# Optimization experiments

Measured on AMD Instinct MI355X. Metric: run time of the kernel, lower is better.

The kernel has to match this reference:

```python
import jax, jax.numpy as jnp
import numpy as np


def setup_inputs() -> dict:
    key = jax.random.key(0)
    k1, k2, k3 = jax.random.split(key, 3)
    B, C, L, D = 2, 8, 256, 128
    start_hidden = jax.random.normal(k1, (B, C, L, D), dtype=jnp.float32)
    end_hidden = jax.random.normal(k2, (B, C, L, D), dtype=jnp.float32)
    # nn.Parameter initialized uniform_(-0.1, 0.1)
    v = jax.random.uniform(k3, (D,), dtype=jnp.float32, minval=-0.1, maxval=0.1)
    return {"start_hidden": start_hidden, "end_hidden": end_hidden, "v": v}


def reference(start_hidden, end_hidden, v):
    # start_hidden: [B, C, L, D], end_hidden: [B, C, L, D], v: [D]
    # additive pairwise scoring: tanh(s_i + e_j) . v  for every (i, j) span
    add_hidden = jnp.tanh(start_hidden[:, :, :, None, :] + end_hidden[:, :, None, :, :])  # [B,C,L,L,D]
    res = jnp.einsum('bcnmd,d->bcnm', add_hidden, v)  # [B, C, L, L]
    span_ner_mat_tensor = jnp.transpose(res, (0, 2, 3, 1))  # [B, L, L, C]
    return span_ner_mat_tensor
```

## Files before the change

### kernel.cpp

```cpp
#include <hip/hip_runtime.h>


#define LDIM 256
#define DDIM 128
#define DPAD 132

__global__ __launch_bounds__(256) void span_tanh_dot_kernel(
    const float* __restrict__ start_h,
    const float* __restrict__ end_h,
    const float* __restrict__ v,
    float* __restrict__ out,
    int C)
{
    __shared__ float s_pool[32 * DPAD];
    __shared__ float e_t[32][DPAD];
    __shared__ float s_vsum;
    float (*s_t)[DPAD] = (float (*)[DPAD])s_pool;

    const int bc = blockIdx.z;
    const int i0 = blockIdx.y * 32;
    const int j0 = blockIdx.x * 32;
    const int tx = threadIdx.x;
    const int ty = threadIdx.y;
    const int g  = threadIdx.z;
    const int t  = ty * 8 + tx;
    const int tid = g * 64 + t;

    const float K = 2.8853900817779268f;

    const float* sg = start_h + ((size_t)bc * LDIM + i0) * DDIM;
    const float* eg = end_h   + ((size_t)bc * LDIM + j0) * DDIM;

    #pragma unroll
    for (int k = 0; k < 4; ++k) {
        const int idx = tid + k * 256;
        const int r  = idx >> 5;
        const int c4 = (idx & 31) << 2;
        const float4 vv = *(const float4*)(v + c4);
        const float w0 = __builtin_amdgcn_rcpf(vv.x);
        const float w1 = __builtin_amdgcn_rcpf(vv.y);
        const float w2 = __builtin_amdgcn_rcpf(vv.z);
        const float w3 = __builtin_amdgcn_rcpf(vv.w);
        float4 a = *(const float4*)(sg + r * DDIM + c4);
        a.x = __builtin_amdgcn_exp2f(K * a.x) * w0;
        a.y = __builtin_amdgcn_exp2f(K * a.y) * w1;
        a.z = __builtin_amdgcn_exp2f(K * a.z) * w2;
        a.w = __builtin_amdgcn_exp2f(K * a.w) * w3;
        *(float4*)(&s_t[r][c4]) = a;
        float4 b = *(const float4*)(eg + r * DDIM + c4);
        b.x = __builtin_amdgcn_exp2f(K * b.x);
        b.y = __builtin_amdgcn_exp2f(K * b.y);
        b.z = __builtin_amdgcn_exp2f(K * b.z);
        b.w = __builtin_amdgcn_exp2f(K * b.w);
        *(float4*)(&e_t[r][c4]) = b;
    }

    if (tid < 128) {
        s_t[tid >> 2][128 + (tid & 3)] = __builtin_amdgcn_rcpf(v[tid]);
    }

    if (g == 0) {
        float2 vv = *(const float2*)(v + 2 * t);
        float p = vv.x + vv.y;
        #pragma unroll
        for (int off = 1; off < 64; off <<= 1) p += __shfl_xor(p, off);
        if (t == 0) s_vsum = p;
    }
    __syncthreads();

    const int g8 = __builtin_amdgcn_readfirstlane(g) * 8;

    float acc00 = 0.f, acc01 = 0.f, acc02 = 0.f, acc03 = 0.f;
    float acc10 = 0.f, acc11 = 0.f, acc12 = 0.f, acc13 = 0.f;
    float acc20 = 0.f, acc21 = 0.f, acc22 = 0.f, acc23 = 0.f;
    float acc30 = 0.f, acc31 = 0.f, acc32 = 0.f, acc33 = 0.f;

#define QUAD(ACC, S, E)                                            \
    {                                                              \
        float u0 = fmaf((S).x, (E).x, W.x);                        \
        float u1 = fmaf((S).y, (E).y, W.y);                        \
        float u2 = fmaf((S).z, (E).z, W.z);                        \
        float u3 = fmaf((S).w, (E).w, W.w);                        \
        float ab = u0 * u1, cd = u2 * u3;                          \
        float n01 = u0 + u1;                                       \
        float n23 = u2 + u3;                                       \
        float N = fmaf(n01, cd, n23 * ab);                         \
        float r = __builtin_amdgcn_rcpf(ab * cd);                  \
        ACC = fmaf(N, r, ACC);                                     \
    }

    #pragma unroll 2
    for (int it = 0; it < 8; ++it) {
        const int d = (g8 + it) * 4;
        const float4 W  = *(const float4*)(&s_t[g8 + it][128]);
        const float4 s0 = *(const float4*)(&s_t[ty     ][d]);
        const float4 s1 = *(const float4*)(&s_t[ty +  8][d]);
        const float4 s2 = *(const float4*)(&s_t[ty + 16][d]);
        const float4 s3 = *(const float4*)(&s_t[ty + 24][d]);
        const float4 e0 = *(const float4*)(&e_t[tx     ][d]);
        const float4 e1 = *(const float4*)(&e_t[tx +  8][d]);
        const float4 e2 = *(const float4*)(&e_t[tx + 16][d]);
        const float4 e3 = *(const float4*)(&e_t[tx + 24][d]);

        QUAD(acc00, s0, e0); QUAD(acc01, s0, e1); QUAD(acc02, s0, e2); QUAD(acc03, s0, e3);
        QUAD(acc10, s1, e0); QUAD(acc11, s1, e1); QUAD(acc12, s1, e2); QUAD(acc13, s1, e3);
        QUAD(acc20, s2, e0); QUAD(acc21, s2, e1); QUAD(acc22, s2, e2); QUAD(acc23, s2, e3);
        QUAD(acc30, s3, e0); QUAD(acc31, s3, e1); QUAD(acc32, s3, e2); QUAD(acc33, s3, e3);
    }
#undef QUAD

    __syncthreads();
    float* red = s_pool;
#define PARK(A, B, ACC) red[(((A) * 4 + (B)) * 4 + g) * 64 + t] = ACC;
    PARK(0,0,acc00) PARK(0,1,acc01) PARK(0,2,acc02) PARK(0,3,acc03)
    PARK(1,0,acc10) PARK(1,1,acc11) PARK(1,2,acc12) PARK(1,3,acc13)
    PARK(2,0,acc20) PARK(2,1,acc21) PARK(2,2,acc22) PARK(2,3,acc23)
    PARK(3,0,acc30) PARK(3,1,acc31) PARK(3,2,acc32) PARK(3,3,acc33)
#undef PARK
    __syncthreads();

#define COMB(B)                                                    \
    (red[((g * 4 + (B)) * 4 + 0) * 64 + t] +                       \
     red[((g * 4 + (B)) * 4 + 1) * 64 + t] +                       \
     red[((g * 4 + (B)) * 4 + 2) * 64 + t] +                       \
     red[((g * 4 + (B)) * 4 + 3) * 64 + t])
    const float o0 = COMB(0);
    const float o1 = COMB(1);
    const float o2 = COMB(2);
    const float o3 = COMB(3);
#undef COMB

    const int b_ = bc / C;
    const int c_ = bc - b_ * C;
    const float Sv = s_vsum;
    const int i = i0 + ty + 8 * g;
    const size_t rowbase = (((size_t)b_ * LDIM + i) * LDIM) * C + c_;
    out[rowbase + (size_t)(j0 + tx     ) * C] = fmaf(-2.f, o0, Sv);
    out[rowbase + (size_t)(j0 + tx +  8) * C] = fmaf(-2.f, o1, Sv);
    out[rowbase + (size_t)(j0 + tx + 16) * C] = fmaf(-2.f, o2, Sv);
    out[rowbase + (size_t)(j0 + tx + 24) * C] = fmaf(-2.f, o3, Sv);
}

extern "C" void kernel_launch(void* const* d_in, const int* in_sizes, int n_in,
                              void* d_out, int out_size, void* d_ws, size_t ws_size,
                              hipStream_t stream) {
    const float* start_h = (const float*)d_in[0];
    const float* end_h   = (const float*)d_in[1];
    const float* v       = (const float*)d_in[2];
    float* out = (float*)d_out;

    const int BC = in_sizes[0] / (LDIM * DDIM);
    const int C  = 8;

    dim3 grid(LDIM / 32, LDIM / 32, BC);
    dim3 block(8, 8, 4);
    span_tanh_dot_kernel<<<grid, block, 0, stream>>>(start_h, end_h, v, out, C);
}
```

Baseline: 18.34 us.

## Enlarge block tile to 64x64 with 1024 threads and fold scaling into W

Each block now covers a 64x64 (i,j) tile using 16 wavefronts arranged as 4 quadrants by 4 D-slices. Each exponentiated start/end row is loaded once per block and reused across twice as many pairs, which cuts redundant global loads and exp work. The -2 output scale and 1/v weights are folded into a separate shared W array, so the epilogue becomes a plain add. The trade-off is a 4x smaller grid (256 blocks) and larger LDS use per block, which may reduce occupancy and latency hiding.

```diff
diff --git a/kernel.cpp b/kernel.cpp
--- a/kernel.cpp
+++ b/kernel.cpp
@@ -5,61 +5,69 @@
 #define DDIM 128
 #define DPAD 132
 
-__global__ __launch_bounds__(256) void span_tanh_dot_kernel(
+__global__ __launch_bounds__(1024) void span_tanh_dot_kernel(
     const float* __restrict__ start_h,
     const float* __restrict__ end_h,
     const float* __restrict__ v,
     float* __restrict__ out,
     int C)
 {
-    __shared__ float s_pool[32 * DPAD];
-    __shared__ float e_t[32][DPAD];
+    __shared__ float pool[2 * 64 * DPAD];
+    __shared__ float W_s[DDIM];
     __shared__ float s_vsum;
-    float (*s_t)[DPAD] = (float (*)[DPAD])s_pool;
+
+    float* s_t = pool;
+    float* e_t = pool + 64 * DPAD;
 
     const int bc = blockIdx.z;
-    const int i0 = blockIdx.y * 32;
-    const int j0 = blockIdx.x * 32;
+    const int i0 = blockIdx.y * 64;
+    const int j0 = blockIdx.x * 64;
     const int tx = threadIdx.x;
     const int ty = threadIdx.y;
-    const int g  = threadIdx.z;
+    const int wz = threadIdx.z;
     const int t  = ty * 8 + tx;
-    const int tid = g * 64 + t;
+    const int tid = wz * 64 + t;
+
+    const int q  = wz & 3;
+    const int h  = wz >> 2;
+    const int qi = q >> 1, qj = q & 1;
 
     const float K = 2.8853900817779268f;
 
     const float* sg = start_h + ((size_t)bc * LDIM + i0) * DDIM;
     const float* eg = end_h   + ((size_t)bc * LDIM + j0) * DDIM;
 
+    if (tid < 32) {
+        const float4 vv = *(const float4*)(v + 4 * tid);
+        float4 w;
+        w.x = -0.5f * __builtin_amdgcn_rcpf(vv.x);
+        w.y = -0.5f * __builtin_amdgcn_rcpf(vv.y);
+        w.z = -0.5f * __builtin_amdgcn_rcpf(vv.z);
+        w.w = -0.5f * __builtin_amdgcn_rcpf(vv.w);
+        *(float4*)(&W_s[4 * tid]) = w;
+    }
+
     #pragma unroll
-    for (int k = 0; k < 4; ++k) {
-        const int idx = tid + k * 256;
+    for (int k = 0; k < 2; ++k) {
+        const int idx = tid + k * 1024;
         const int r  = idx >> 5;
         const int c4 = (idx & 31) << 2;
         const float4 vv = *(const float4*)(v + c4);
-        const float w0 = __builtin_amdgcn_rcpf(vv.x);
-        const float w1 = __builtin_amdgcn_rcpf(vv.y);
-        const float w2 = __builtin_amdgcn_rcpf(vv.z);
-        const float w3 = __builtin_amdgcn_rcpf(vv.w);
         float4 a = *(const float4*)(sg + r * DDIM + c4);
-        a.x = __builtin_amdgcn_exp2f(K * a.x) * w0;
-        a.y = __builtin_amdgcn_exp2f(K * a.y) * w1;
-        a.z = __builtin_amdgcn_exp2f(K * a.z) * w2;
-        a.w = __builtin_amdgcn_exp2f(K * a.w) * w3;
-        *(float4*)(&s_t[r][c4]) = a;
+        a.x = __builtin_amdgcn_exp2f(K * a.x) * (-0.5f * __builtin_amdgcn_rcpf(vv.x));
+        a.y = __builtin_amdgcn_exp2f(K * a.y) * (-0.5f * __builtin_amdgcn_rcpf(vv.y));
+        a.z = __builtin_amdgcn_exp2f(K * a.z) * (-0.5f * __builtin_amdgcn_rcpf(vv.z));
+        a.w = __builtin_amdgcn_exp2f(K * a.w) * (-0.5f * __builtin_amdgcn_rcpf(vv.w));
+        *(float4*)(&s_t[r * DPAD + c4]) = a;
         float4 b = *(const float4*)(eg + r * DDIM + c4);
         b.x = __builtin_amdgcn_exp2f(K * b.x);
         b.y = __builtin_amdgcn_exp2f(K * b.y);
         b.z = __builtin_amdgcn_exp2f(K * b.z);
         b.w = __builtin_amdgcn_exp2f(K * b.w);
-        *(float4*)(&e_t[r][c4]) = b;
+        *(float4*)(&e_t[r * DPAD + c4]) = b;
     }
 
-    if (tid < 128) {
-        s_t[tid >> 2][128 + (tid & 3)] = __builtin_amdgcn_rcpf(v[tid]);
-    }
-
-    if (g == 0) {
+    if (wz == 0) {
         float2 vv = *(const float2*)(v + 2 * t);
         float p = vv.x + vv.y;
         #pragma unroll
@@ -68,7 +76,9 @@
     }
     __syncthreads();
 
-    const int g8 = __builtin_amdgcn_readfirstlane(g) * 8;
+    const int dbase = __builtin_amdgcn_readfirstlane(h) * 32;
+    const float* srow = s_t + (qi * 32 + ty) * DPAD;
+    const float* erow = e_t + (qj * 32 + tx) * DPAD;
 
     float acc00 = 0.f, acc01 = 0.f, acc02 = 0.f, acc03 = 0.f;
     float acc10 = 0.f, acc11 = 0.f, acc12 = 0.f, acc13 = 0.f;
@@ -91,16 +101,16 @@
 
     #pragma unroll 2
     for (int it = 0; it < 8; ++it) {
-        const int d = (g8 + it) * 4;
-        const float4 W  = *(const float4*)(&s_t[g8 + it][128]);
-        const float4 s0 = *(const float4*)(&s_t[ty     ][d]);
-        const float4 s1 = *(const float4*)(&s_t[ty +  8][d]);
-        const float4 s2 = *(const float4*)(&s_t[ty + 16][d]);
-        const float4 s3 = *(const float4*)(&s_t[ty + 24][d]);
-        const float4 e0 = *(const float4*)(&e_t[tx     ][d]);
-        const float4 e1 = *(const float4*)(&e_t[tx +  8][d]);
-        const float4 e2 = *(const float4*)(&e_t[tx + 16][d]);
-        const float4 e3 = *(const float4*)(&e_t[tx + 24][d]);
+        const int d = dbase + it * 4;
+        const float4 W  = *(const float4*)(&W_s[d]);
+        const float4 s0 = *(const float4*)(srow + d);
+        const float4 s1 = *(const float4*)(srow +  8 * DPAD + d);
+        const float4 s2 = *(const float4*)(srow + 16 * DPAD + d);
+        const float4 s3 = *(const float4*)(srow + 24 * DPAD + d);
+        const float4 e0 = *(const float4*)(erow + d);
+        const float4 e1 = *(const float4*)(erow +  8 * DPAD + d);
+        const float4 e2 = *(const float4*)(erow + 16 * DPAD + d);
+        const float4 e3 = *(const float4*)(erow + 24 * DPAD + d);
 
         QUAD(acc00, s0, e0); QUAD(acc01, s0, e1); QUAD(acc02, s0, e2); QUAD(acc03, s0, e3);
         QUAD(acc10, s1, e0); QUAD(acc11, s1, e1); QUAD(acc12, s1, e2); QUAD(acc13, s1, e3);
@@ -110,20 +120,20 @@
 #undef QUAD
 
     __syncthreads();
-    float* red = s_pool;
-#define PARK(A, B, ACC) red[(((A) * 4 + (B)) * 4 + g) * 64 + t] = ACC;
-    PARK(0,0,acc00) PARK(0,1,acc01) PARK(0,2,acc02) PARK(0,3,acc03)
-    PARK(1,0,acc10) PARK(1,1,acc11) PARK(1,2,acc12) PARK(1,3,acc13)
-    PARK(2,0,acc20) PARK(2,1,acc21) PARK(2,2,acc22) PARK(2,3,acc23)
-    PARK(3,0,acc30) PARK(3,1,acc31) PARK(3,2,acc32) PARK(3,3,acc33)
-#undef PARK
+    float* park = pool;
+#define PK(A, B, ACC) park[((((q * 4 + h) * 4 + (A)) * 4 + (B)) * 64) + t] = ACC;
+    PK(0,0,acc00) PK(0,1,acc01) PK(0,2,acc02) PK(0,3,acc03)
+    PK(1,0,acc10) PK(1,1,acc11) PK(1,2,acc12) PK(1,3,acc13)
+    PK(2,0,acc20) PK(2,1,acc21) PK(2,2,acc22) PK(2,3,acc23)
+    PK(3,0,acc30) PK(3,1,acc31) PK(3,2,acc32) PK(3,3,acc33)
+#undef PK
     __syncthreads();
 
-#define COMB(B)                                                    \
-    (red[((g * 4 + (B)) * 4 + 0) * 64 + t] +                       \
-     red[((g * 4 + (B)) * 4 + 1) * 64 + t] +                       \
-     red[((g * 4 + (B)) * 4 + 2) * 64 + t] +                       \
-     red[((g * 4 + (B)) * 4 + 3) * 64 + t])
+#define COMB(B)                                                        \
+    (park[(((q * 4 + 0) * 4 + h) * 4 + (B)) * 64 + t] +                \
+     park[(((q * 4 + 1) * 4 + h) * 4 + (B)) * 64 + t] +                \
+     park[(((q * 4 + 2) * 4 + h) * 4 + (B)) * 64 + t] +                \
+     park[(((q * 4 + 3) * 4 + h) * 4 + (B)) * 64 + t])
     const float o0 = COMB(0);
     const float o1 = COMB(1);
     const float o2 = COMB(2);
@@ -133,12 +143,13 @@
     const int b_ = bc / C;
     const int c_ = bc - b_ * C;
     const float Sv = s_vsum;
-    const int i = i0 + ty + 8 * g;
+    const int i = i0 + qi * 32 + ty + 8 * h;
+    const int j = j0 + qj * 32 + tx;
     const size_t rowbase = (((size_t)b_ * LDIM + i) * LDIM) * C + c_;
-    out[rowbase + (size_t)(j0 + tx     ) * C] = fmaf(-2.f, o0, Sv);
-    out[rowbase + (size_t)(j0 + tx +  8) * C] = fmaf(-2.f, o1, Sv);
-    out[rowbase + (size_t)(j0 + tx + 16) * C] = fmaf(-2.f, o2, Sv);
-    out[rowbase + (size_t)(j0 + tx + 24) * C] = fmaf(-2.f, o3, Sv);
+    out[rowbase + (size_t)(j     ) * C] = Sv + o0;
+    out[rowbase + (size_t)(j +  8) * C] = Sv + o1;
+    out[rowbase + (size_t)(j + 16) * C] = Sv + o2;
+    out[rowbase + (size_t)(j + 24) * C] = Sv + o3;
 }
 
 extern "C" void kernel_launch(void* const* d_in, const int* in_sizes, int n_in,
@@ -152,7 +163,7 @@
     const int BC = in_sizes[0] / (LDIM * DDIM);
     const int C  = 8;
 
-    dim3 grid(LDIM / 32, LDIM / 32, BC);
-    dim3 block(8, 8, 4);
+    dim3 grid(LDIM / 64, LDIM / 64, BC);
+    dim3 block(8, 8, 16);
     span_tanh_dot_kernel<<<grid, block, 0, stream>>>(start_h, end_h, v, out, C);
 }
```

Result: slower. 19.55 us (+6.6%).

## Precompute exp tables in workspace and read them directly from global memory

Applied to the files above, without the earlier changes.

Adds a precompute kernel that writes exp(2x)/v-scaled start and exp(2x) end tables into the workspace, once per element instead of once per tile. The main kernel then drops its shared-memory staging and reads float4 operands straight from global/L2, and folds the -2 scaling into the weights. This removes the redundant exp work and one barrier, at the cost of an extra launch and about 4 MB of extra global traffic. Per-thread global loads in the inner loop may also have higher latency than LDS reads. A fallback kernel keeps the shared-memory path for when no workspace is available.

```diff
diff --git a/kernel.cpp b/kernel.cpp
--- a/kernel.cpp
+++ b/kernel.cpp
@@ -3,19 +3,49 @@
 
 #define LDIM 256
 #define DDIM 128
-#define DPAD 132
-
-__global__ __launch_bounds__(256) void span_tanh_dot_kernel(
-    const float* __restrict__ start_h,
-    const float* __restrict__ end_h,
+#define TBL_ELEMS (2 * 8 * 256 * 128)
+#define KLOG2E 2.8853900817779268f
+
+__global__ __launch_bounds__(256) void precompute_kernel(
+    const float* __restrict__ s_in,
+    const float* __restrict__ e_in,
+    const float* __restrict__ v,
+    float* __restrict__ ws)
+{
+    const int i = blockIdx.x * 256 + threadIdx.x;
+    const int c4 = (i & 31) << 2;
+    const float4 vv = *(const float4*)(v + c4);
+    const float w0 = -0.5f * __builtin_amdgcn_rcpf(vv.x);
+    const float w1 = -0.5f * __builtin_amdgcn_rcpf(vv.y);
+    const float w2 = -0.5f * __builtin_amdgcn_rcpf(vv.z);
+    const float w3 = -0.5f * __builtin_amdgcn_rcpf(vv.w);
+
+    float4 a = *(const float4*)(s_in + 4 * (size_t)i);
+    float4 o;
+    o.x = __builtin_amdgcn_exp2f(KLOG2E * a.x) * w0;
+    o.y = __builtin_amdgcn_exp2f(KLOG2E * a.y) * w1;
+    o.z = __builtin_amdgcn_exp2f(KLOG2E * a.z) * w2;
+    o.w = __builtin_amdgcn_exp2f(KLOG2E * a.w) * w3;
+    *(float4*)(ws + 4 * (size_t)i) = o;
+
+    float4 b = *(const float4*)(e_in + 4 * (size_t)i);
+    float4 p;
+    p.x = __builtin_amdgcn_exp2f(KLOG2E * b.x);
+    p.y = __builtin_amdgcn_exp2f(KLOG2E * b.y);
+    p.z = __builtin_amdgcn_exp2f(KLOG2E * b.z);
+    p.w = __builtin_amdgcn_exp2f(KLOG2E * b.w);
+    *(float4*)(ws + TBL_ELEMS + 4 * (size_t)i) = p;
+}
+
+__global__ __launch_bounds__(256) void span_main_kernel(
+    const float* __restrict__ ws,
     const float* __restrict__ v,
     float* __restrict__ out,
     int C)
 {
-    __shared__ float s_pool[32 * DPAD];
-    __shared__ float e_t[32][DPAD];
+    __shared__ float red[4096];
+    __shared__ float W_s[DDIM];
     __shared__ float s_vsum;
-    float (*s_t)[DPAD] = (float (*)[DPAD])s_pool;
 
     const int bc = blockIdx.z;
     const int i0 = blockIdx.y * 32;
@@ -26,39 +56,15 @@
     const int t  = ty * 8 + tx;
     const int tid = g * 64 + t;
 
-    const float K = 2.8853900817779268f;
-
-    const float* sg = start_h + ((size_t)bc * LDIM + i0) * DDIM;
-    const float* eg = end_h   + ((size_t)bc * LDIM + j0) * DDIM;
-
-    #pragma unroll
-    for (int k = 0; k < 4; ++k) {
-        const int idx = tid + k * 256;
-        const int r  = idx >> 5;
-        const int c4 = (idx & 31) << 2;
-        const float4 vv = *(const float4*)(v + c4);
-        const float w0 = __builtin_amdgcn_rcpf(vv.x);
-        const float w1 = __builtin_amdgcn_rcpf(vv.y);
-        const float w2 = __builtin_amdgcn_rcpf(vv.z);
-        const float w3 = __builtin_amdgcn_rcpf(vv.w);
-        float4 a = *(const float4*)(sg + r * DDIM + c4);
-        a.x = __builtin_amdgcn_exp2f(K * a.x) * w0;
-        a.y = __builtin_amdgcn_exp2f(K * a.y) * w1;
-        a.z = __builtin_amdgcn_exp2f(K * a.z) * w2;
-        a.w = __builtin_amdgcn_exp2f(K * a.w) * w3;
-        *(float4*)(&s_t[r][c4]) = a;
-        float4 b = *(const float4*)(eg + r * DDIM + c4);
-        b.x = __builtin_amdgcn_exp2f(K * b.x);
-        b.y = __builtin_amdgcn_exp2f(K * b.y);
-        b.z = __builtin_amdgcn_exp2f(K * b.z);
-        b.w = __builtin_amdgcn_exp2f(K * b.w);
-        *(float4*)(&e_t[r][c4]) = b;
-    }
-
-    if (tid < 128) {
-        s_t[tid >> 2][128 + (tid & 3)] = __builtin_amdgcn_rcpf(v[tid]);
-    }
-
+    if (tid < 32) {
+        const float4 vv = *(const float4*)(v + 4 * tid);
+        float4 w;
+        w.x = -0.5f * __builtin_amdgcn_rcpf(vv.x);
+        w.y = -0.5f * __builtin_amdgcn_rcpf(vv.y);
+        w.z = -0.5f * __builtin_amdgcn_rcpf(vv.z);
+        w.w = -0.5f * __builtin_amdgcn_rcpf(vv.w);
+        *(float4*)(&W_s[4 * tid]) = w;
+    }
     if (g == 0) {
         float2 vv = *(const float2*)(v + 2 * t);
         float p = vv.x + vv.y;
@@ -68,7 +74,9 @@
     }
     __syncthreads();
 
-    const int g8 = __builtin_amdgcn_readfirstlane(g) * 8;
+    const int dbase = __builtin_amdgcn_readfirstlane(g) * 32;
+    const float* Sb = ws + (size_t)bc * (LDIM * DDIM) + (i0 + ty) * DDIM;
+    const float* Eb = ws + TBL_ELEMS + (size_t)bc * (LDIM * DDIM) + (j0 + tx) * DDIM;
 
     float acc00 = 0.f, acc01 = 0.f, acc02 = 0.f, acc03 = 0.f;
     float acc10 = 0.f, acc11 = 0.f, acc12 = 0.f, acc13 = 0.f;
@@ -91,16 +99,16 @@
 
     #pragma unroll 2
     for (int it = 0; it < 8; ++it) {
-        const int d = (g8 + it) * 4;
-        const float4 W  = *(const float4*)(&s_t[g8 + it][128]);
-        const float4 s0 = *(const float4*)(&s_t[ty     ][d]);
-        const float4 s1 = *(const float4*)(&s_t[ty +  8][d]);
-        const float4 s2 = *(const float4*)(&s_t[ty + 16][d]);
-        const float4 s3 = *(const float4*)(&s_t[ty + 24][d]);
-        const float4 e0 = *(const float4*)(&e_t[tx     ][d]);
-        const float4 e1 = *(const float4*)(&e_t[tx +  8][d]);
-        const float4 e2 = *(const float4*)(&e_t[tx + 16][d]);
-        const float4 e3 = *(const float4*)(&e_t[tx + 24][d]);
+        const int d = dbase + it * 4;
+        const float4 s0 = *(const float4*)(Sb + d);
+        const float4 s1 = *(const float4*)(Sb +  8 * DDIM + d);
+        const float4 s2 = *(const float4*)(Sb + 16 * DDIM + d);
+        const float4 s3 = *(const float4*)(Sb + 24 * DDIM + d);
+        const float4 e0 = *(const float4*)(Eb + d);
+        const float4 e1 = *(const float4*)(Eb +  8 * DDIM + d);
+        const float4 e2 = *(const float4*)(Eb + 16 * DDIM + d);
+        const float4 e3 = *(const float4*)(Eb + 24 * DDIM + d);
+        const float4 W  = *(const float4*)(&W_s[d]);
 
         QUAD(acc00, s0, e0); QUAD(acc01, s0, e1); QUAD(acc02, s0, e2); QUAD(acc03, s0, e3);
         QUAD(acc10, s1, e0); QUAD(acc11, s1, e1); QUAD(acc12, s1, e2); QUAD(acc13, s1, e3);
@@ -109,8 +117,6 @@
     }
 #undef QUAD
 
-    __syncthreads();
-    float* red = s_pool;
 #define PARK(A, B, ACC) red[(((A) * 4 + (B)) * 4 + g) * 64 + t] = ACC;
     PARK(0,0,acc00) PARK(0,1,acc01) PARK(0,2,acc02) PARK(0,3,acc03)
     PARK(1,0,acc10) PARK(1,1,acc11) PARK(1,2,acc12) PARK(1,3,acc13)
@@ -135,10 +141,138 @@
     const float Sv = s_vsum;
     const int i = i0 + ty + 8 * g;
     const size_t rowbase = (((size_t)b_ * LDIM + i) * LDIM) * C + c_;
-    out[rowbase + (size_t)(j0 + tx     ) * C] = fmaf(-2.f, o0, Sv);
-    out[rowbase + (size_t)(j0 + tx +  8) * C] = fmaf(-2.f, o1, Sv);
-    out[rowbase + (size_t)(j0 + tx + 16) * C] = fmaf(-2.f, o2, Sv);
-    out[rowbase + (size_t)(j0 + tx + 24) * C] = fmaf(-2.f, o3, Sv);
+    out[rowbase + (size_t)(j0 + tx     ) * C] = Sv + o0;
+    out[rowbase + (size_t)(j0 + tx +  8) * C] = Sv + o1;
+    out[rowbase + (size_t)(j0 + tx + 16) * C] = Sv + o2;
+    out[rowbase + (size_t)(j0 + tx + 24) * C] = Sv + o3;
+}
+
+#define DPAD 132
+
+__global__ __launch_bounds__(256) void span_fallback_kernel(
+    const float* __restrict__ start_h,
+    const float* __restrict__ end_h,
+    const float* __restrict__ v,
+    float* __restrict__ out,
+    int C)
+{
+    __shared__ float s_pool[32 * DPAD];
+    __shared__ float e_t[32][DPAD];
+    __shared__ float s_vsum;
+    float (*s_t)[DPAD] = (float (*)[DPAD])s_pool;
+
+    const int bc = blockIdx.z;
+    const int i0 = blockIdx.y * 32;
+    const int j0 = blockIdx.x * 32;
+    const int tx = threadIdx.x, ty = threadIdx.y, g = threadIdx.z;
+    const int t = ty * 8 + tx;
+    const int tid = g * 64 + t;
+
+    const float* sg = start_h + ((size_t)bc * LDIM + i0) * DDIM;
+    const float* eg = end_h   + ((size_t)bc * LDIM + j0) * DDIM;
+
+    #pragma unroll
+    for (int k = 0; k < 4; ++k) {
+        const int idx = tid + k * 256;
+        const int r  = idx >> 5;
+        const int c4 = (idx & 31) << 2;
+        const float4 vv = *(const float4*)(v + c4);
+        float4 a = *(const float4*)(sg + r * DDIM + c4);
+        a.x = __builtin_amdgcn_exp2f(KLOG2E * a.x) * (-0.5f * __builtin_amdgcn_rcpf(vv.x));
+        a.y = __builtin_amdgcn_exp2f(KLOG2E * a.y) * (-0.5f * __builtin_amdgcn_rcpf(vv.y));
+        a.z = __builtin_amdgcn_exp2f(KLOG2E * a.z) * (-0.5f * __builtin_amdgcn_rcpf(vv.z));
+        a.w = __builtin_amdgcn_exp2f(KLOG2E * a.w) * (-0.5f * __builtin_amdgcn_rcpf(vv.w));
+        *(float4*)(&s_t[r][c4]) = a;
+        float4 b = *(const float4*)(eg + r * DDIM + c4);
+        b.x = __builtin_amdgcn_exp2f(KLOG2E * b.x);
+        b.y = __builtin_amdgcn_exp2f(KLOG2E * b.y);
+        b.z = __builtin_amdgcn_exp2f(KLOG2E * b.z);
+        b.w = __builtin_amdgcn_exp2f(KLOG2E * b.w);
+        *(float4*)(&e_t[r][c4]) = b;
+    }
+    if (g == 0) {
+        float2 vv = *(const float2*)(v + 2 * t);
+        float p = vv.x + vv.y;
+        #pragma unroll
+        for (int off = 1; off < 64; off <<= 1) p += __shfl_xor(p, off);
+        if (t == 0) s_vsum = p;
+    }
+    __syncthreads();
+
+    const int dbase = __builtin_amdgcn_readfirstlane(g) * 32;
+    float acc00 = 0.f, acc01 = 0.f, acc02 = 0.f, acc03 = 0.f;
+    float acc10 = 0.f, acc11 = 0.f, acc12 = 0.f, acc13 = 0.f;
+    float acc20 = 0.f, acc21 = 0.f, acc22 = 0.f, acc23 = 0.f;
+    float acc30 = 0.f, acc31 = 0.f, acc32 = 0.f, acc33 = 0.f;
+
+#define QUAD(ACC, S, E, WV)                                        \
+    {                                                              \
+        float u0 = fmaf((S).x, (E).x, (WV).x);                     \
+        float u1 = fmaf((S).y, (E).y, (WV).y);                     \
+        float u2 = fmaf((S).z, (E).z, (WV).z);                     \
+        float u3 = fmaf((S).w, (E).w, (WV).w);                     \
+        float ab = u0 * u1, cd = u2 * u3;                          \
+        float n01 = u0 + u1;                                       \
+        float n23 = u2 + u3;                                       \
+        float N = fmaf(n01, cd, n23 * ab);                         \
+        float r = __builtin_amdgcn_rcpf(ab * cd);                  \
+        ACC = fmaf(N, r, ACC);                                     \
+    }
+
+    #pragma unroll 2
+    for (int it = 0; it < 8; ++it) {
+        const int d = dbase + it * 4;
+        const float4 vv = *(const float4*)(v + d);
+        float4 W;
+        W.x = -0.5f * __builtin_amdgcn_rcpf(vv.x);
+        W.y = -0.5f * __builtin_amdgcn_rcpf(vv.y);
+        W.z = -0.5f * __builtin_amdgcn_rcpf(vv.z);
+        W.w = -0.5f * __builtin_amdgcn_rcpf(vv.w);
+        const float4 s0 = *(const float4*)(&s_t[ty     ][d]);
+        const float4 s1 = *(const float4*)(&s_t[ty +  8][d]);
+        const float4 s2 = *(const float4*)(&s_t[ty + 16][d]);
+        const float4 s3 = *(const float4*)(&s_t[ty + 24][d]);
+        const float4 e0 = *(const float4*)(&e_t[tx     ][d]);
+        const float4 e1 = *(const float4*)(&e_t[tx +  8][d]);
+        const float4 e2 = *(const float4*)(&e_t[tx + 16][d]);
+        const float4 e3 = *(const float4*)(&e_t[tx + 24][d]);
+
+        QUAD(acc00, s0, e0, W); QUAD(acc01, s0, e1, W); QUAD(acc02, s0, e2, W); QUAD(acc03, s0, e3, W);
+        QUAD(acc10, s1, e0, W); QUAD(acc11, s1, e1, W); QUAD(acc12, s1, e2, W); QUAD(acc13, s1, e3, W);
+        QUAD(acc20, s2, e0, W); QUAD(acc21, s2, e1, W); QUAD(acc22, s2, e2, W); QUAD(acc23, s2, e3, W);
+        QUAD(acc30, s3, e0, W); QUAD(acc31, s3, e1, W); QUAD(acc32, s3, e2, W); QUAD(acc33, s3, e3, W);
+    }
+#undef QUAD
+
+    __syncthreads();
+    float* red = s_pool;
+#define PARK(A, B, ACC) red[(((A) * 4 + (B)) * 4 + g) * 64 + t] = ACC;
+    PARK(0,0,acc00) PARK(0,1,acc01) PARK(0,2,acc02) PARK(0,3,acc03)
+    PARK(1,0,acc10) PARK(1,1,acc11) PARK(1,2,acc12) PARK(1,3,acc13)
+    PARK(2,0,acc20) PARK(2,1,acc21) PARK(2,2,acc22) PARK(2,3,acc23)
+    PARK(3,0,acc30) PARK(3,1,acc31) PARK(3,2,acc32) PARK(3,3,acc33)
+#undef PARK
+    __syncthreads();
+#define COMB(B)                                                    \
+    (red[((g * 4 + (B)) * 4 + 0) * 64 + t] +                       \
+     red[((g * 4 + (B)) * 4 + 1) * 64 + t] +                       \
+     red[((g * 4 + (B)) * 4 + 2) * 64 + t] +                       \
+     red[((g * 4 + (B)) * 4 + 3) * 64 + t])
+    const float o0 = COMB(0);
+    const float o1 = COMB(1);
+    const float o2 = COMB(2);
+    const float o3 = COMB(3);
+#undef COMB
+
+    const int b_ = bc / C;
+    const int c_ = bc - b_ * C;
+    const float Sv = s_vsum;
+    const int i = i0 + ty + 8 * g;
+    const size_t rowbase = (((size_t)b_ * LDIM + i) * LDIM) * C + c_;
+    out[rowbase + (size_t)(j0 + tx     ) * C] = Sv + o0;
+    out[rowbase + (size_t)(j0 + tx +  8) * C] = Sv + o1;
+    out[rowbase + (size_t)(j0 + tx + 16) * C] = Sv + o2;
+    out[rowbase + (size_t)(j0 + tx + 24) * C] = Sv + o3;
 }
 
 extern "C" void kernel_launch(void* const* d_in, const int* in_sizes, int n_in,
@@ -151,8 +285,17 @@
 
     const int BC = in_sizes[0] / (LDIM * DDIM);
     const int C  = 8;
-
-    dim3 grid(LDIM / 32, LDIM / 32, BC);
-    dim3 block(8, 8, 4);
-    span_tanh_dot_kernel<<<grid, block, 0, stream>>>(start_h, end_h, v, out, C);
+    const size_t ws_needed = (size_t)2 * TBL_ELEMS * sizeof(float);
+
+    if (ws_size >= ws_needed && d_ws != nullptr) {
+        float* ws = (float*)d_ws;
+        precompute_kernel<<<TBL_ELEMS / 4 / 256, 256, 0, stream>>>(start_h, end_h, v, ws);
+        dim3 grid(LDIM / 32, LDIM / 32, BC);
+        dim3 block(8, 8, 4);
+        span_main_kernel<<<grid, block, 0, stream>>>(ws, v, out, C);
+    } else {
+        dim3 grid(LDIM / 32, LDIM / 32, BC);
+        dim3 block(8, 8, 4);
+        span_fallback_kernel<<<grid, block, 0, stream>>>(start_h, end_h, v, out, C);
+    }
 }
```

Result: slower. 33.42 us (+82.2%).
